# Performance work log

Measured on AMD Instinct MI355X. Metric: run time of the kernel, lower is better.

## Reference

```python
import jax, jax.numpy as jnp
import numpy as np
from jax import lax

L, B, V, E, H, T = 256, 256, 50000, 300, 256, 17


def setup_inputs() -> dict:
    key = jax.random.key(0)
    ks = jax.random.split(key, 17)
    words = jax.random.randint(ks[0], (L, B), 0, V, dtype=jnp.int32)
    tags = jax.random.randint(ks[1], (L, B), 0, T, dtype=jnp.int32)
    lengths = jax.random.randint(ks[2], (B,), L // 2, L + 1)
    # time-major mask; mask[0] must be all-on (torchcrf requirement)
    mask = (jnp.arange(L)[:, None] < lengths[None, :]).astype(jnp.int32)

    def u(k, shape, scale):
        return jax.random.uniform(k, shape, jnp.float32, -scale, scale)

    sc = 1.0 / np.sqrt(H)  # pytorch LSTM init scale
    embed_table = jax.random.normal(ks[3], (V, E), jnp.float32)
    w_ih_f = u(ks[4], (4 * H, E), sc); w_hh_f = u(ks[5], (4 * H, H), sc)
    b_ih_f = u(ks[6], (4 * H,), sc);   b_hh_f = u(ks[7], (4 * H,), sc)
    w_ih_b = u(ks[8], (4 * H, E), sc); w_hh_b = u(ks[9], (4 * H, H), sc)
    b_ih_b = u(ks[10], (4 * H,), sc);  b_hh_b = u(ks[11], (4 * H,), sc)
    lin_w = u(ks[12], (T, 2 * H), np.sqrt(6.0 / (T + 2 * H)))  # xavier_uniform
    lin_b = u(ks[13], (T,), np.sqrt(6.0 / (T + 1)))
    start_trans = u(ks[14], (T,), 0.1)
    end_trans = u(ks[15], (T,), 0.1)
    trans = u(ks[16], (T, T), 0.1)
    return dict(words=words, tags=tags, mask=mask, embed_table=embed_table,
                w_ih_f=w_ih_f, w_hh_f=w_hh_f, b_ih_f=b_ih_f, b_hh_f=b_hh_f,
                w_ih_b=w_ih_b, w_hh_b=w_hh_b, b_ih_b=b_ih_b, b_hh_b=b_hh_b,
                lin_w=lin_w, lin_b=lin_b, start_trans=start_trans,
                end_trans=end_trans, trans=trans)


def _lstm_dir(x, w_ih, w_hh, b_ih, b_hh, reverse):
    # x: (L, B, E) -> hidden outputs (L, B, H); pytorch gate order i,f,g,o
    Bn = x.shape[1]
    Hn = w_hh.shape[1]
    bias = b_ih + b_hh

    def step(carry, xt):
        h, c = carry
        gates = xt @ w_ih.T + h @ w_hh.T + bias
        i, f, g, o = jnp.split(gates, 4, axis=-1)
        c = jax.nn.sigmoid(f) * c + jax.nn.sigmoid(i) * jnp.tanh(g)
        h = jax.nn.sigmoid(o) * jnp.tanh(c)
        return (h, c), h

    init = (jnp.zeros((Bn, Hn), x.dtype), jnp.zeros((Bn, Hn), x.dtype))
    _, hs = lax.scan(step, init, x, reverse=reverse)
    return hs


def _crf_nll(emissions, tags, mask, start_trans, end_trans, trans):
    # emissions: (L,B,T), tags/mask: (L,B); torchcrf log-likelihood, reduction='sum'
    mf = mask.astype(emissions.dtype)
    barange = jnp.arange(emissions.shape[1])
    # numerator (gold path score), fully vectorized
    em_t = jnp.take_along_axis(emissions, tags[..., None], axis=-1)[..., 0]  # (L,B)
    trans_t = trans[tags[:-1], tags[1:]]  # (L-1,B)
    score = start_trans[tags[0]] + em_t[0]
    score = score + jnp.sum((trans_t + em_t[1:]) * mf[1:], axis=0)
    seq_ends = jnp.sum(mask, axis=0) - 1  # (B,)
    last_tags = tags[seq_ends, barange]
    score = score + end_trans[last_tags]
    # denominator (log-partition) via forward-algorithm scan
    def step(alpha, inp):
        em_i, m_i = inp  # (B,T), (B,)
        nxt = jax.scipy.special.logsumexp(
            alpha[:, :, None] + trans[None] + em_i[:, None, :], axis=1)
        alpha = jnp.where(m_i[:, None] > 0, nxt, alpha)
        return alpha, None

    alpha0 = start_trans[None, :] + emissions[0]  # (B,T)
    alpha, _ = lax.scan(step, alpha0, (emissions[1:], mask[1:]))
    logZ = jax.scipy.special.logsumexp(alpha + end_trans[None, :], axis=-1)
    llh = jnp.sum(score - logZ)
    return -llh


def reference(words, tags, mask, embed_table,
              w_ih_f, w_hh_f, b_ih_f, b_hh_f,
              w_ih_b, w_hh_b, b_ih_b, b_hh_b,
              lin_w, lin_b, start_trans, end_trans, trans):
    embed = jnp.take(embed_table, words, axis=0)  # (L,B,E); dropout = identity (eval)
    h_f = _lstm_dir(embed, w_ih_f, w_hh_f, b_ih_f, b_hh_f, reverse=False)
    h_b = _lstm_dir(embed, w_ih_b, w_hh_b, b_ih_b, b_hh_b, reverse=True)
    lstm_out = jnp.concatenate([h_f, h_b], axis=-1)  # (L,B,2H)
    emissions = lstm_out @ lin_w.T + lin_b  # (L,B,T)
    return _crf_nll(emissions, tags, mask, start_trans, end_trans, trans)
```

## Files before the change

kernel.cpp:

```cpp
#include <hip/hip_runtime.h>

#define L_ 256
#define B_ 256
#define V_ 50000
#define E_ 300
#define H_ 256
#define T_ 17
#define G4 1024

typedef short short8 __attribute__((ext_vector_type(8)));
typedef float f32x4 __attribute__((ext_vector_type(4)));
typedef float f32x2 __attribute__((ext_vector_type(2)));
typedef unsigned long long ull;

static __device__ __forceinline__ short f2bf(float x) {
    unsigned int u = __float_as_uint(x);
    u = (u + 0x7fffu + ((u >> 16) & 1u)) >> 16;
    return (short)u;
}
static __device__ __forceinline__ float bf2f(unsigned int u) {
    return __uint_as_float(u << 16);
}

#if __has_builtin(__builtin_amdgcn_exp2f)
#define EXP2(x) __builtin_amdgcn_exp2f(x)
#else
#define EXP2(x) __expf(0.6931471805599453f * (x))
#endif
#if __has_builtin(__builtin_amdgcn_rcpf)
#define RCP(x) __builtin_amdgcn_rcpf(x)
#else
#define RCP(x) (1.0f / (x))
#endif

static __device__ __forceinline__ float sigm(float x) {
    return RCP(1.0f + EXP2(-1.4426950408889634f * x));
}
static __device__ __forceinline__ float tanh_(float x) {
    return fmaf(-2.0f, RCP(EXP2(2.8853900817779268f * x) + 1.0f), 1.0f);
}

static __device__ __forceinline__ unsigned int f2fp8(float x) {
    float ax = fminf(fabsf(x), 448.0f);
    int e = (int)(__float_as_uint(ax) >> 23) - 127;
    int ec = e < -6 ? -6 : e;
    float sc = __uint_as_float((unsigned int)(130 - ec) << 23);
    float t = __builtin_fmaf(ax, sc, 12582912.0f);
    int n = (int)(__float_as_uint(t) & 0x3fffff);
    int code = ((ec + 7) << 3) + n - 8;
    return (unsigned int)code | ((__float_as_uint(x) >> 24) & 0x80);
}
static __device__ __forceinline__ unsigned int pk_fp8(float a, float b) {
#if __has_builtin(__builtin_amdgcn_cvt_pk_fp8_f32)
    return (unsigned int)__builtin_amdgcn_cvt_pk_fp8_f32(a, b, 0, false) & 0xffffu;
#else
    return f2fp8(a) | (f2fp8(b) << 8);
#endif
}
static __device__ __forceinline__ float dec8(unsigned int b) {
    unsigned int f = ((b & 0x7fu) << 20) + 0x3C000000u;
    f |= (b & 0x80u) << 24;
    return __uint_as_float(f);
}
template <bool HI>
static __device__ __forceinline__ f32x2 pk_f32(unsigned int u) {
#if __has_builtin(__builtin_amdgcn_cvt_pk_f32_fp8)
    return __builtin_amdgcn_cvt_pk_f32_fp8((int)u, HI);
#else
    f32x2 r;
    r.x = dec8((u >> (HI ? 16 : 0)) & 0xff);
    r.y = dec8((u >> (HI ? 24 : 8)) & 0xff);
    return r;
#endif
}

static __device__ __forceinline__ unsigned int pk2bf(float x, float y) {
#if __has_builtin(__builtin_amdgcn_perm)
    return __builtin_amdgcn_perm(__float_as_uint(y) + 0x8000u,
                                 __float_as_uint(x) + 0x8000u, 0x07060302u);
#else
    return (unsigned int)(unsigned short)f2bf(x) |
           ((unsigned int)(unsigned short)f2bf(y) << 16);
#endif
}
static __device__ __forceinline__ short8 pack8(float4 a, float4 b) {
    union { unsigned int u[4]; short8 s; } r;
    r.u[0] = pk2bf(a.x, a.y);
    r.u[1] = pk2bf(a.z, a.w);
    r.u[2] = pk2bf(b.x, b.y);
    r.u[3] = pk2bf(b.z, b.w);
    return r.s;
}

__global__ __launch_bounds__(256) void prep_all(const float* __restrict__ whf,
                                                const float* __restrict__ whb,
                                                const float* __restrict__ lin_w,
                                                unsigned char* __restrict__ wB8,
                                                unsigned char* __restrict__ linB8) {
    int gid = blockIdx.x * 256 + threadIdx.x;
    if (gid < 524288) {
        int j = gid & 7;
        int lane = (gid >> 3) & 63;
        int gt = (gid >> 9) & 3;
        int kt = (gid >> 11) & 7;
        int wv = (gid >> 14) & 15;
        int dir = gid >> 18;
        int g = gt * 256 + wv * 16 + (lane & 15);
        int k = kt * 32 + (lane >> 4) * 8 + j;
        const float* w = dir ? whb : whf;
        wB8[gid] = (unsigned char)f2fp8(w[g * H_ + k] * 8.0f);
    } else {
        int i2 = gid - 524288;
        int dir = (i2 >> 13) & 1;
        int wv = (i2 >> 12) & 1;
        int kt = (i2 >> 9) & 7;
        int lane = (i2 >> 3) & 63;
        int j = i2 & 7;
        int t = wv * 16 + (lane & 15);
        int k = kt * 32 + (lane >> 4) * 8 + j;
        float v = (t < T_) ? lin_w[t * (2 * H_) + dir * H_ + k] * 32.0f : 0.0f;
        linB8[i2] = (unsigned char)f2fp8(v);
    }
}

__global__ __launch_bounds__(256) void prep_bih(const float* __restrict__ w_ih_f,
                                                const float* __restrict__ w_ih_b,
                                                unsigned short* __restrict__ dstf,
                                                unsigned short* __restrict__ dstb) {
    int gid = blockIdx.x * 256 + threadIdx.x;
    int dir = gid >= 327680;
    int i = gid - dir * 327680;
    int gtile = i / 5120;
    int r = i - gtile * 5120;
    int kt = r >> 9;
    int lane = (r >> 3) & 63;
    int j = r & 7;
    int g = gtile * 16 + (lane & 15);
    int k = kt * 32 + (lane >> 4) * 8 + j;
    const float* src = dir ? w_ih_b : w_ih_f;
    unsigned short* dst = dir ? dstb : dstf;
    dst[i] = (unsigned short)((k < E_) ? f2bf(src[g * E_ + k]) : (short)0);
}

__global__ __launch_bounds__(512, 2) void tg_gemm(const float* __restrict__ table,
                                                  const unsigned short* __restrict__ wBihF,
                                                  const unsigned short* __restrict__ wBihB,
                                                  const float* __restrict__ b_ih_f,
                                                  const float* __restrict__ b_hh_f,
                                                  const float* __restrict__ b_ih_b,
                                                  const float* __restrict__ b_hh_b,
                                                  unsigned char* __restrict__ tg8) {
    __shared__ __align__(16) unsigned short Bs[2][16][512];
    const int tid = threadIdx.x;
    const int w = tid >> 6;
    const int lane = tid & 63;
    const int n = lane & 15;
    const int q = lane >> 4;
    const int jt0 = blockIdx.y * 2;
    const int v0 = blockIdx.x * 256 + w * 32;

    const int r0 = v0 + n;
    const int r1 = v0 + 16 + n;
    const float* arow0 = table + (size_t)(r0 < V_ ? r0 : V_ - 1) * E_;
    const float* arow1 = table + (size_t)(r1 < V_ ? r1 : V_ - 1) * E_;

    const unsigned short* bsrc[2];
#pragma unroll
    for (int s = 0; s < 2; ++s) {
        const int f = w + s * 8;
        const int dir = f >> 3, jj = (f >> 2) & 1, gt = f & 3;
        const int gtile = gt * 16 + jt0 + jj;
        bsrc[s] = (dir ? wBihB : wBihF) + (size_t)gtile * 5120 + lane * 8;
    }

    f32x4 acc[2][4][2][2];
#pragma unroll
    for (int jj = 0; jj < 2; ++jj)
#pragma unroll
        for (int gt = 0; gt < 4; ++gt)
#pragma unroll
            for (int rt = 0; rt < 2; ++rt)
#pragma unroll
                for (int d = 0; d < 2; ++d)
                    acc[jj][gt][rt][d] = (f32x4){0.f, 0.f, 0.f, 0.f};

    short8 bpre[2];
    bpre[0] = *(const short8*)bsrc[0];
    bpre[1] = *(const short8*)bsrc[1];
    float4 apre[4];
    {
        const int e0 = q * 8;
        apre[0] = *(const float4*)(arow0 + e0);
        apre[1] = *(const float4*)(arow0 + e0 + 4);
        apre[2] = *(const float4*)(arow1 + e0);
        apre[3] = *(const float4*)(arow1 + e0 + 4);
    }

#pragma unroll 1
    for (int kt = 0; kt < 10; ++kt) {
        const int buf = kt & 1;
        *(short8*)&Bs[buf][w][lane * 8] = bpre[0];
        *(short8*)&Bs[buf][w + 8][lane * 8] = bpre[1];
        __syncthreads();

        const short8 af0 = pack8(apre[0], apre[1]);
        const short8 af1 = pack8(apre[2], apre[3]);

        if (kt < 9) {
            const int e0n = (kt + 1) * 32 + q * 8;
            if (kt + 1 < 9) {
                apre[0] = *(const float4*)(arow0 + e0n);
                apre[1] = *(const float4*)(arow0 + e0n + 4);
                apre[2] = *(const float4*)(arow1 + e0n);
                apre[3] = *(const float4*)(arow1 + e0n + 4);
            } else {
                float va[8], vb[8];
#pragma unroll
                for (int j = 0; j < 8; ++j) {
                    const int e = e0n + j;
                    va[j] = (e < E_) ? arow0[e] : 0.0f;
                    vb[j] = (e < E_) ? arow1[e] : 0.0f;
                }
                apre[0] = (float4){va[0], va[1], va[2], va[3]};
                apre[1] = (float4){va[4], va[5], va[6], va[7]};
                apre[2] = (float4){vb[0], vb[1], vb[2], vb[3]};
                apre[3] = (float4){vb[4], vb[5], vb[6], vb[7]};
            }
            bpre[0] = *(const short8*)(bsrc[0] + (kt + 1) * 512);
            bpre[1] = *(const short8*)(bsrc[1] + (kt + 1) * 512);
        }

#pragma unroll
        for (int f = 0; f < 16; ++f) {
            const int dir = f >> 3, jj = (f >> 2) & 1, gt = f & 3;
            const short8 bf = *(const short8*)&Bs[buf][f][lane * 8];
            acc[jj][gt][0][dir] = __builtin_amdgcn_mfma_f32_16x16x32_bf16(af0, bf, acc[jj][gt][0][dir], 0, 0, 0);
            acc[jj][gt][1][dir] = __builtin_amdgcn_mfma_f32_16x16x32_bf16(af1, bf, acc[jj][gt][1][dir], 0, 0, 0);
        }
    }

    float bias[2][2][4];
#pragma unroll
    for (int d = 0; d < 2; ++d)
#pragma unroll
        for (int jj = 0; jj < 2; ++jj)
#pragma unroll
            for (int gt = 0; gt < 4; ++gt) {
                const int g = gt * 256 + (jt0 + jj) * 16 + n;
                bias[d][jj][gt] = d ? (b_ih_b[g] + b_hh_b[g]) : (b_ih_f[g] + b_hh_f[g]);
            }

#pragma unroll
    for (int d = 0; d < 2; ++d) {
        unsigned int* tgd = (unsigned int*)(tg8 + (size_t)d * 51200000);
#pragma unroll
        for (int jj = 0; jj < 2; ++jj) {
            const int dcol = (jt0 + jj) * 16 + n;
#pragma unroll
            for (int rt = 0; rt < 2; ++rt) {
#pragma unroll
                for (int r = 0; r < 4; ++r) {
                    const int v = v0 + rt * 16 + q * 4 + r;
                    if (v < V_) {
                        const float x0 = (acc[jj][0][rt][d][r] + bias[d][jj][0]) * 64.0f;
                        const float x1 = (acc[jj][1][rt][d][r] + bias[d][jj][1]) * 64.0f;
                        const float x2 = (acc[jj][2][rt][d][r] + bias[d][jj][2]) * 64.0f;
                        const float x3 = (acc[jj][3][rt][d][r] + bias[d][jj][3]) * 64.0f;
                        tgd[(size_t)v * 256 + dcol] = pk_fp8(x0, x1) | (pk_fp8(x2, x3) << 16);
                    }
                }
            }
        }
    }
}

__global__ __launch_bounds__(1024, 4) void lstm_fp8(const unsigned char* __restrict__ tg8,
                                                    const ull* __restrict__ wB8,
                                                    const int* __restrict__ words,
                                                    const ull* __restrict__ linB8,
                                                    unsigned short* __restrict__ emf,
                                                    unsigned short* __restrict__ emb) {
    __shared__ __align__(16) unsigned char hbuf[2][16][264];
    const int tid = threadIdx.x;
    const int wv = tid >> 6;
    const int lane = tid & 63;
    const int n = lane & 15;
    const int q = lane >> 4;
    const int dir = blockIdx.x >> 4;
    const int b0 = (blockIdx.x & 15) * 16;

    for (int i = tid; i < 2 * 16 * 264; i += 1024) (&hbuf[0][0][0])[i] = 0;
    __syncthreads();

    float cst[4] = {0.f, 0.f, 0.f, 0.f};

    const int l0 = dir ? (L_ - 1) : 0;
    const int dl = dir ? -1 : 1;

    ull wfrag[32];
    {
        const ull* wbase = wB8 + (size_t)dir * 32768 + (size_t)wv * 2048 + lane;
#pragma unroll
        for (int i = 0; i < 32; ++i) wfrag[i] = wbase[i * 64];
    }

    const unsigned char* tgd = tg8 + (size_t)dir * 51200000;
    const unsigned int laneoff = wv * 64 + n * 4;
    unsigned short* emx = dir ? emb : emf;
    const ull* lfrag = linB8 + (size_t)(dir * 2 + wv) * 512 + lane;
    const int t_em = wv * 16 + n;

    const float kSig = -1.4426950408889634f / 64.0f;
    const float kTanh = 2.8853900817779268f / 64.0f;

    unsigned int tgr[4];
    int4 wnxt;
    {
        const int4 w04 = *(const int4*)&words[l0 * B_ + b0 + q * 4];
        tgr[0] = *(const unsigned int*)(tgd + (((unsigned)w04.x << 10) + laneoff));
        tgr[1] = *(const unsigned int*)(tgd + (((unsigned)w04.y << 10) + laneoff));
        tgr[2] = *(const unsigned int*)(tgd + (((unsigned)w04.z << 10) + laneoff));
        tgr[3] = *(const unsigned int*)(tgd + (((unsigned)w04.w << 10) + laneoff));
        wnxt = *(const int4*)&words[(l0 + dl) * B_ + b0 + q * 4];
    }

    int p = 0;
    for (int step = 0; step < L_; ++step) {
        const int l = l0 + dl * step;
        f32x4 acc[4];
#pragma unroll
        for (int r = 0; r < 4; ++r) {
            f32x2 p0 = pk_f32<false>(tgr[r]);
            f32x2 p1 = pk_f32<true>(tgr[r]);
            acc[0][r] = p0.x; acc[1][r] = p0.y; acc[2][r] = p1.x; acc[3][r] = p1.y;
        }

        if (step + 1 < L_) {
            tgr[0] = *(const unsigned int*)(tgd + (((unsigned)wnxt.x << 10) + laneoff));
            tgr[1] = *(const unsigned int*)(tgd + (((unsigned)wnxt.y << 10) + laneoff));
            tgr[2] = *(const unsigned int*)(tgd + (((unsigned)wnxt.z << 10) + laneoff));
            tgr[3] = *(const unsigned int*)(tgd + (((unsigned)wnxt.w << 10) + laneoff));
        }
        int4 wtmp = {0, 0, 0, 0};
        if (step + 2 < L_) {
            wtmp = *(const int4*)&words[(l + 2 * dl) * B_ + b0 + q * 4];
        }

#pragma unroll
        for (int kt = 0; kt < 8; ++kt) {
            const ull af = *(const ull*)&hbuf[p][n][kt * 32 + q * 8];
#pragma unroll
            for (int gt = 0; gt < 4; ++gt)
                acc[gt] = __builtin_amdgcn_mfma_f32_16x16x32_fp8_fp8(
                    (long long)af, (long long)wfrag[kt * 4 + gt], acc[gt], 0, 0, 0);
        }

        float hv[4];
#pragma unroll
        for (int r = 0; r < 4; ++r) {
            const float ig = RCP(1.0f + EXP2(acc[0][r] * kSig));
            const float fg = RCP(1.0f + EXP2(acc[1][r] * kSig));
            const float gg = fmaf(-2.0f, RCP(EXP2(acc[2][r] * kTanh) + 1.0f), 1.0f);
            const float og = RCP(1.0f + EXP2(acc[3][r] * kSig));
            const float cn = fmaf(fg, cst[r], ig * gg);
            cst[r] = cn;
            hv[r] = og * tanh_(cn);
        }
        {
            const unsigned int p01 = pk_fp8(hv[0] * 8.0f, hv[1] * 8.0f);
            const unsigned int p23 = pk_fp8(hv[2] * 8.0f, hv[3] * 8.0f);
            hbuf[p ^ 1][q * 4 + 0][wv * 16 + n] = (unsigned char)(p01 & 0xff);
            hbuf[p ^ 1][q * 4 + 1][wv * 16 + n] = (unsigned char)(p01 >> 8);
            hbuf[p ^ 1][q * 4 + 2][wv * 16 + n] = (unsigned char)(p23 & 0xff);
            hbuf[p ^ 1][q * 4 + 3][wv * 16 + n] = (unsigned char)(p23 >> 8);
        }
        __syncthreads();

        if (wv < 2) {
            f32x4 eacc = (f32x4){0.f, 0.f, 0.f, 0.f};
#pragma unroll
            for (int kt = 0; kt < 8; ++kt) {
                const ull af = *(const ull*)&hbuf[p ^ 1][n][kt * 32 + q * 8];
                eacc = __builtin_amdgcn_mfma_f32_16x16x32_fp8_fp8(
                    (long long)af, (long long)lfrag[kt * 64], eacc, 0, 0, 0);
            }
            if (t_em < T_) {
                const size_t embase = ((size_t)l * B_ + b0) * T_ + t_em + (size_t)q * 4 * T_;
#pragma unroll
                for (int r = 0; r < 4; ++r)
                    emx[embase + r * T_] = (unsigned short)f2bf(eacc[r] * (1.0f / 256.0f));
            }
        }

        wnxt = wtmp;
        p ^= 1;
    }
}

__global__ __launch_bounds__(64) void crf_kernel(const unsigned short* __restrict__ emf,
                                                 const unsigned short* __restrict__ emb,
                                                 const int* __restrict__ tags,
                                                 const int* __restrict__ mask,
                                                 const float* __restrict__ start_trans,
                                                 const float* __restrict__ end_trans,
                                                 const float* __restrict__ trans,
                                                 const float* __restrict__ lin_b,
                                                 float* __restrict__ llh) {
    const int b = blockIdx.x;
    const int t = threadIdx.x;
    __shared__ float tr[T_ * T_];
    __shared__ float lb[T_];
    for (int i = t; i < T_ * T_; i += 64) tr[i] = trans[i];
    if (t < T_) lb[t] = lin_b[t];
    __syncthreads();

    const int tc = (t < T_) ? t : (T_ - 1);
    const float lbc = lb[tc];
    float trc[T_];
#pragma unroll
    for (int s = 0; s < T_; ++s) trc[s] = tr[s * T_ + tc];

    float part = 0.0f;
    int msum = 0;
    for (int l = t; l < L_; l += 64) {
        const int idx = l * B_ + b;
        const int m = mask[idx];
        msum += m;
        const int tl = tags[idx];
        const float emt = bf2f(emf[(size_t)idx * T_ + tl]) + bf2f(emb[(size_t)idx * T_ + tl]) + lb[tl];
        if (l == 0) {
            part += start_trans[tl] + emt;
        } else {
            const int tp = tags[(l - 1) * B_ + b];
            part += m ? (tr[tp * T_ + tl] + emt) : 0.0f;
        }
    }
    for (int o = 32; o; o >>= 1) {
        part += __shfl_down(part, o);
        msum += __shfl_down(msum, o);
    }
    const int len = __shfl(msum, 0);

    float alpha = start_trans[tc] + bf2f(emf[(size_t)b * T_ + tc]) + bf2f(emb[(size_t)b * T_ + tc]) + lbc;
    float env = 0.0f;
    if (len > 1) {
        const size_t i1 = ((size_t)B_ + b) * T_ + tc;
        env = bf2f(emf[i1]) + bf2f(emb[i1]) + lbc;
    }
    for (int l = 1; l < len; ++l) {
        const float cur = env;
        if (l + 1 < len) {
            const size_t ix = ((size_t)(l + 1) * B_ + b) * T_ + tc;
            env = bf2f(emf[ix]) + bf2f(emb[ix]) + lbc;
        }
        float mx = -1e30f;
#pragma unroll
        for (int s = 0; s < T_; ++s) {
            const float as = __shfl(alpha, s);
            mx = fmaxf(mx, as + trc[s]);
        }
        float sm = 0.0f;
#pragma unroll
        for (int s = 0; s < T_; ++s) {
            const float as = __shfl(alpha, s);
            sm += __expf(as + trc[s] - mx);
        }
        alpha = mx + __logf(sm) + cur;
    }
    float val = (t < T_) ? (alpha + end_trans[t]) : -1e30f;
    float mx = val;
    for (int o = 32; o; o >>= 1) mx = fmaxf(mx, __shfl_down(mx, o));
    const float mx_all = __shfl(mx, 0);
    float sm = __expf(val - mx_all);
    for (int o = 32; o; o >>= 1) sm += __shfl_down(sm, o);

    if (t == 0) {
        const float score = part + end_trans[tags[(len - 1) * B_ + b]];
        const float logZ = mx_all + __logf(sm);
        llh[b] = score - logZ;
    }
}

__global__ __launch_bounds__(256) void final_reduce(const float* __restrict__ llh,
                                                    float* __restrict__ out) {
    const int t = threadIdx.x;
    float v = llh[t];
    for (int o = 32; o; o >>= 1) v += __shfl_down(v, o);
    __shared__ float wsum[4];
    if ((t & 63) == 0) wsum[t >> 6] = v;
    __syncthreads();
    if (t == 0) out[0] = -(wsum[0] + wsum[1] + wsum[2] + wsum[3]);
}

extern "C" void kernel_launch(void* const* d_in, const int* in_sizes, int n_in,
                              void* d_out, int out_size, void* d_ws, size_t ws_size,
                              hipStream_t stream) {
    const int* words = (const int*)d_in[0];
    const int* tags = (const int*)d_in[1];
    const int* mask = (const int*)d_in[2];
    const float* table = (const float*)d_in[3];
    const float* w_ih_f = (const float*)d_in[4];
    const float* w_hh_f = (const float*)d_in[5];
    const float* b_ih_f = (const float*)d_in[6];
    const float* b_hh_f = (const float*)d_in[7];
    const float* w_ih_b = (const float*)d_in[8];
    const float* w_hh_b = (const float*)d_in[9];
    const float* b_ih_b = (const float*)d_in[10];
    const float* b_hh_b = (const float*)d_in[11];
    const float* lin_w = (const float*)d_in[12];
    const float* lin_b = (const float*)d_in[13];
    const float* start_trans = (const float*)d_in[14];
    const float* end_trans = (const float*)d_in[15];
    const float* trans = (const float*)d_in[16];

    char* ws = (char*)d_ws;
    unsigned char* tg8 = (unsigned char*)ws;
    unsigned char* wB8 = (unsigned char*)(ws + 102400000);
    unsigned char* linB8 = (unsigned char*)(ws + 102924288);
    unsigned short* emf = (unsigned short*)(ws + 102940672);
    unsigned short* emb = (unsigned short*)(ws + 105168896);
    float* llh = (float*)(ws + 107397120);
    unsigned short* wBihF = emf;
    unsigned short* wBihB = emb;

    prep_all<<<2112, 256, 0, stream>>>(w_hh_f, w_hh_b, lin_w, wB8, linB8);
    prep_bih<<<2560, 256, 0, stream>>>(w_ih_f, w_ih_b, wBihF, wBihB);

    tg_gemm<<<dim3(196, 8), 512, 0, stream>>>(table, wBihF, wBihB,
                                              b_ih_f, b_hh_f, b_ih_b, b_hh_b, tg8);

    lstm_fp8<<<32, 1024, 0, stream>>>(tg8, (const ull*)wB8, words, (const ull*)linB8, emf, emb);

    crf_kernel<<<256, 64, 0, stream>>>(emf, emb, tags, mask, start_trans, end_trans, trans, lin_b, llh);
    final_reduce<<<1, 256, 0, stream>>>(llh, (float*)d_out);
}
```

Baseline: 915.0 us.

## Merge weight prep kernels, deepen tg_gemm prefetch, use LDS-only barriers

Three changes. The two weight-preparation kernels are merged into one launch, saving one kernel launch. The input-projection GEMM now prefetches global A/B tiles two k-steps ahead instead of one, to hide more memory latency, at the cost of more registers. Some __syncthreads are replaced with an inline-asm barrier that waits only on LDS counters, avoiding waits on outstanding global loads; this relies on the asm being correct for ordering.

```diff
diff --git a/kernel.cpp b/kernel.cpp
--- a/kernel.cpp
+++ b/kernel.cpp
@@ -12,6 +12,8 @@
 typedef float f32x4 __attribute__((ext_vector_type(4)));
 typedef float f32x2 __attribute__((ext_vector_type(2)));
 typedef unsigned long long ull;
+
+#define BARRIER_LDS() asm volatile("s_waitcnt lgkmcnt(0)\n\ts_barrier" ::: "memory")
 
 static __device__ __forceinline__ short f2bf(float x) {
     unsigned int u = __float_as_uint(x);
@@ -92,11 +94,15 @@
     return r.s;
 }
 
-__global__ __launch_bounds__(256) void prep_all(const float* __restrict__ whf,
-                                                const float* __restrict__ whb,
-                                                const float* __restrict__ lin_w,
-                                                unsigned char* __restrict__ wB8,
-                                                unsigned char* __restrict__ linB8) {
+__global__ __launch_bounds__(256) void prep_w(const float* __restrict__ whf,
+                                              const float* __restrict__ whb,
+                                              const float* __restrict__ lin_w,
+                                              const float* __restrict__ w_ih_f,
+                                              const float* __restrict__ w_ih_b,
+                                              unsigned char* __restrict__ wB8,
+                                              unsigned char* __restrict__ linB8,
+                                              unsigned short* __restrict__ wBihF,
+                                              unsigned short* __restrict__ wBihB) {
     int gid = blockIdx.x * 256 + threadIdx.x;
     if (gid < 524288) {
         int j = gid & 7;
@@ -109,7 +115,7 @@
         int k = kt * 32 + (lane >> 4) * 8 + j;
         const float* w = dir ? whb : whf;
         wB8[gid] = (unsigned char)f2fp8(w[g * H_ + k] * 8.0f);
-    } else {
+    } else if (gid < 540672) {
         int i2 = gid - 524288;
         int dir = (i2 >> 13) & 1;
         int wv = (i2 >> 12) & 1;
@@ -120,26 +126,21 @@
         int k = kt * 32 + (lane >> 4) * 8 + j;
         float v = (t < T_) ? lin_w[t * (2 * H_) + dir * H_ + k] * 32.0f : 0.0f;
         linB8[i2] = (unsigned char)f2fp8(v);
-    }
-}
-
-__global__ __launch_bounds__(256) void prep_bih(const float* __restrict__ w_ih_f,
-                                                const float* __restrict__ w_ih_b,
-                                                unsigned short* __restrict__ dstf,
-                                                unsigned short* __restrict__ dstb) {
-    int gid = blockIdx.x * 256 + threadIdx.x;
-    int dir = gid >= 327680;
-    int i = gid - dir * 327680;
-    int gtile = i / 5120;
-    int r = i - gtile * 5120;
-    int kt = r >> 9;
-    int lane = (r >> 3) & 63;
-    int j = r & 7;
-    int g = gtile * 16 + (lane & 15);
-    int k = kt * 32 + (lane >> 4) * 8 + j;
-    const float* src = dir ? w_ih_b : w_ih_f;
-    unsigned short* dst = dir ? dstb : dstf;
-    dst[i] = (unsigned short)((k < E_) ? f2bf(src[g * E_ + k]) : (short)0);
+    } else {
+        int i3 = gid - 540672;
+        int dir = i3 >= 327680;
+        int i = i3 - dir * 327680;
+        int gtile = i / 5120;
+        int r = i - gtile * 5120;
+        int kt = r >> 9;
+        int lane = (r >> 3) & 63;
+        int j = r & 7;
+        int g = gtile * 16 + (lane & 15);
+        int k = kt * 32 + (lane >> 4) * 8 + j;
+        const float* src = dir ? w_ih_b : w_ih_f;
+        unsigned short* dst = dir ? wBihB : wBihF;
+        dst[i] = (unsigned short)((k < E_) ? f2bf(src[g * E_ + k]) : (short)0);
+    }
 }
 
 __global__ __launch_bounds__(512, 2) void tg_gemm(const float* __restrict__ table,
@@ -184,35 +185,37 @@
                 for (int d = 0; d < 2; ++d)
                     acc[jj][gt][rt][d] = (f32x4){0.f, 0.f, 0.f, 0.f};
 
-    short8 bpre[2];
-    bpre[0] = *(const short8*)bsrc[0];
-    bpre[1] = *(const short8*)bsrc[1];
-    float4 apre[4];
-    {
-        const int e0 = q * 8;
-        apre[0] = *(const float4*)(arow0 + e0);
-        apre[1] = *(const float4*)(arow0 + e0 + 4);
-        apre[2] = *(const float4*)(arow1 + e0);
-        apre[3] = *(const float4*)(arow1 + e0 + 4);
+    float4 apre[2][4];
+    short8 bpre[2][2];
+#pragma unroll
+    for (int s = 0; s < 2; ++s) {
+        const int e0 = s * 32 + q * 8;
+        apre[s][0] = *(const float4*)(arow0 + e0);
+        apre[s][1] = *(const float4*)(arow0 + e0 + 4);
+        apre[s][2] = *(const float4*)(arow1 + e0);
+        apre[s][3] = *(const float4*)(arow1 + e0 + 4);
+        bpre[s][0] = *(const short8*)(bsrc[0] + s * 512);
+        bpre[s][1] = *(const short8*)(bsrc[1] + s * 512);
     }
 
 #pragma unroll 1
     for (int kt = 0; kt < 10; ++kt) {
-        const int buf = kt & 1;
-        *(short8*)&Bs[buf][w][lane * 8] = bpre[0];
-        *(short8*)&Bs[buf][w + 8][lane * 8] = bpre[1];
-        __syncthreads();
-
-        const short8 af0 = pack8(apre[0], apre[1]);
-        const short8 af1 = pack8(apre[2], apre[3]);
-
-        if (kt < 9) {
-            const int e0n = (kt + 1) * 32 + q * 8;
-            if (kt + 1 < 9) {
-                apre[0] = *(const float4*)(arow0 + e0n);
-                apre[1] = *(const float4*)(arow0 + e0n + 4);
-                apre[2] = *(const float4*)(arow1 + e0n);
-                apre[3] = *(const float4*)(arow1 + e0n + 4);
+        const int cur = kt & 1;
+        *(short8*)&Bs[cur][w][lane * 8] = bpre[cur][0];
+        *(short8*)&Bs[cur][w + 8][lane * 8] = bpre[cur][1];
+        BARRIER_LDS();
+
+        const short8 af0 = pack8(apre[cur][0], apre[cur][1]);
+        const short8 af1 = pack8(apre[cur][2], apre[cur][3]);
+
+        if (kt + 2 < 10) {
+            const int ktn = kt + 2;
+            const int e0n = ktn * 32 + q * 8;
+            if (ktn < 9) {
+                apre[cur][0] = *(const float4*)(arow0 + e0n);
+                apre[cur][1] = *(const float4*)(arow0 + e0n + 4);
+                apre[cur][2] = *(const float4*)(arow1 + e0n);
+                apre[cur][3] = *(const float4*)(arow1 + e0n + 4);
             } else {
                 float va[8], vb[8];
 #pragma unroll
@@ -221,19 +224,19 @@
                     va[j] = (e < E_) ? arow0[e] : 0.0f;
                     vb[j] = (e < E_) ? arow1[e] : 0.0f;
                 }
-                apre[0] = (float4){va[0], va[1], va[2], va[3]};
-                apre[1] = (float4){va[4], va[5], va[6], va[7]};
-                apre[2] = (float4){vb[0], vb[1], vb[2], vb[3]};
-                apre[3] = (float4){vb[4], vb[5], vb[6], vb[7]};
+                apre[cur][0] = (float4){va[0], va[1], va[2], va[3]};
+                apre[cur][1] = (float4){va[4], va[5], va[6], va[7]};
+                apre[cur][2] = (float4){vb[0], vb[1], vb[2], vb[3]};
+                apre[cur][3] = (float4){vb[4], vb[5], vb[6], vb[7]};
             }
-            bpre[0] = *(const short8*)(bsrc[0] + (kt + 1) * 512);
-            bpre[1] = *(const short8*)(bsrc[1] + (kt + 1) * 512);
+            bpre[cur][0] = *(const short8*)(bsrc[0] + ktn * 512);
+            bpre[cur][1] = *(const short8*)(bsrc[1] + ktn * 512);
         }
 
 #pragma unroll
         for (int f = 0; f < 16; ++f) {
             const int dir = f >> 3, jj = (f >> 2) & 1, gt = f & 3;
-            const short8 bf = *(const short8*)&Bs[buf][f][lane * 8];
+            const short8 bf = *(const short8*)&Bs[cur][f][lane * 8];
             acc[jj][gt][0][dir] = __builtin_amdgcn_mfma_f32_16x16x32_bf16(af0, bf, acc[jj][gt][0][dir], 0, 0, 0);
             acc[jj][gt][1][dir] = __builtin_amdgcn_mfma_f32_16x16x32_bf16(af1, bf, acc[jj][gt][1][dir], 0, 0, 0);
         }
@@ -374,7 +377,7 @@
             hbuf[p ^ 1][q * 4 + 2][wv * 16 + n] = (unsigned char)(p23 & 0xff);
             hbuf[p ^ 1][q * 4 + 3][wv * 16 + n] = (unsigned char)(p23 >> 8);
         }
-        __syncthreads();
+        BARRIER_LDS();
 
         if (wv < 2) {
             f32x4 eacc = (f32x4){0.f, 0.f, 0.f, 0.f};
@@ -523,8 +526,8 @@
     unsigned short* wBihF = emf;
     unsigned short* wBihB = emb;
 
-    prep_all<<<2112, 256, 0, stream>>>(w_hh_f, w_hh_b, lin_w, wB8, linB8);
-    prep_bih<<<2560, 256, 0, stream>>>(w_ih_f, w_ih_b, wBihF, wBihB);
+    prep_w<<<4672, 256, 0, stream>>>(w_hh_f, w_hh_b, lin_w, w_ih_f, w_ih_b,
+                                     wB8, linB8, wBihF, wBihB);
 
     tg_gemm<<<dim3(196, 8), 512, 0, stream>>>(table, wBihF, wBihB,
                                               b_ih_f, b_hh_f, b_ih_b, b_hh_b, tg8);
```

Result: slower. 1.848 ms (+102.0%).
